# Kernel optimization log

Hardware: AMD Instinct MI355X
Metric: run time of the kernel (lower is better)

Reference implementation:

```python
import jax, jax.numpy as jnp
import numpy as np


def setup_inputs() -> dict:
    key = jax.random.key(0)
    k1, k2, k3 = jax.random.split(key, 3)
    S, B, H, D = 1024, 32, 512, 1024  # max_len, batch, bin_rnn_size, bin_rep_size
    hidden = jax.random.normal(k1, (2, B, H), dtype=jnp.float32)
    encoder_outputs = jax.random.normal(k2, (S, B, D), dtype=jnp.float32)
    # nn.Linear(D, D) params; scale W for numerically sane softmax logits
    W = jax.random.normal(k3, (D, D), dtype=jnp.float32) / np.float32(np.sqrt(D))
    b = jnp.zeros((D,), dtype=jnp.float32)
    return {"hidden": hidden, "encoder_outputs": encoder_outputs, "W": W, "b": b}


def reference(hidden, encoder_outputs, W, b):
    # method == 'general'
    B = hidden.shape[1]
    # torch.reshape((-1, B, 2H)).squeeze() == C-order flatten -> [B, 2H]
    h = hidden.reshape(B, -1)                                   # [B, D]
    energy = jnp.einsum('sbd,ed->sbe', encoder_outputs, W) + b  # Linear: x @ W.T + b
    # batch_product_luong + sum over features == contraction
    attn_energies = jnp.einsum('bd,sbd->bs', h, energy)         # [B, S]
    alpha = jax.nn.softmax(attn_energies, axis=1)[:, None, :]   # [B, 1, S]
    # alpha.bmm(encoder_outputs.transpose(0,1)) -> [B, 1, D]
    reps = jnp.einsum('bos,sbd->bod', alpha, encoder_outputs)
    return (reps, alpha)
```

## Files before the change

kernel.cpp:

```cpp
#include <hip/hip_runtime.h>

#define S 1024
#define B 32
#define D 1024
#define NCH 32
#define CH (S / NCH)
#define RPW (CH / 4)
#define NPAIR (RPW / 2)
#define ECH 8
#define EC 128

#define PG_OFF   0
#define G_OFF    (PG_OFF + ECH * B * D)
#define LOG_OFF  (G_OFF + B * D)
#define MARR_OFF (LOG_OFF + B * S)
#define LARR_OFF (MARR_OFF + NCH * B)
#define PACC_OFF (LARR_OFF + NCH * B)

__global__ __launch_bounds__(256) void kA(const float* __restrict__ hid,
                                          const float* __restrict__ W,
                                          float* __restrict__ ws) {
    const int tid = threadIdx.x;
    const int ec = blockIdx.x >> 5;
    const int dc = blockIdx.x & 31;
    __shared__ float h_sh[EC * 33];
    #pragma unroll
    for (int k = 0; k < (EC * B) / 256; ++k) {
        int lin = tid + k * 256;
        int b = lin >> 7;
        int e = lin & (EC - 1);
        h_sh[e * 33 + b] = hid[b * D + ec * EC + e];
    }
    __syncthreads();

    const int dq = tid & 7;
    const int b  = tid >> 3;
    const float4* W4 = (const float4*)W;
    float4 a4 = {0.f, 0.f, 0.f, 0.f};
    for (int e = 0; e < EC; ++e) {
        float h  = h_sh[e * 33 + b];
        float4 w = W4[((size_t)(ec * EC + e) * D + dc * 32) / 4 + dq];
        a4.x += h * w.x; a4.y += h * w.y; a4.z += h * w.z; a4.w += h * w.w;
    }
    float* pg = ws + PG_OFF;
    ((float4*)(pg + (size_t)(ec * B + b) * D + dc * 32))[dq] = a4;
}

__global__ __launch_bounds__(256) void kA2(float* __restrict__ ws) {
    const int idx = blockIdx.x * 256 + threadIdx.x;
    const float4* pg4 = (const float4*)(ws + PG_OFF);
    float4 s4 = {0.f, 0.f, 0.f, 0.f};
    #pragma unroll
    for (int ec = 0; ec < ECH; ++ec) {
        float4 v = pg4[(size_t)ec * (B * D / 4) + idx];
        s4.x += v.x; s4.y += v.y; s4.z += v.z; s4.w += v.w;
    }
    ((float4*)(ws + G_OFF))[idx] = s4;
}

__global__ __launch_bounds__(256) void kB(const float* __restrict__ enc,
                                          float* __restrict__ ws) {
    const int tid  = threadIdx.x;
    const int lane = tid & 63;
    const int wid  = tid >> 6;
    const int c    = blockIdx.x;
    const int b    = blockIdx.y;

    const float* g = ws + G_OFF;
    float* logits = ws + LOG_OFF;
    float* marr   = ws + MARR_OFF;
    float* larr   = ws + LARR_OFF;
    float* pacc   = ws + PACC_OFF;

    __shared__ float4 sacc[4 * 256];
    __shared__ float sm[4], sl[4];

    const float4* encb = (const float4*)enc;
    const int row0 = c * CH + wid * RPW;
    const size_t rstride = (size_t)B * (D / 4);
    size_t base = ((size_t)row0 * B + b) * (D / 4) + lane;

    float4 cur[8], nxt[8];
    #pragma unroll
    for (int j = 0; j < 4; ++j) {
        cur[j]     = encb[base + j * 64];
        cur[4 + j] = encb[base + rstride + j * 64];
    }
    #pragma unroll
    for (int j = 0; j < 4; ++j) {
        nxt[j]     = encb[base + 2 * rstride + j * 64];
        nxt[4 + j] = encb[base + 3 * rstride + j * 64];
    }
    float4 gv[4];
    #pragma unroll
    for (int j = 0; j < 4; ++j)
        gv[j] = ((const float4*)(g + b * D))[j * 64 + lane];

    float m = -3.0e38f, l = 0.f;
    float4 acc[4] = {{0,0,0,0},{0,0,0,0},{0,0,0,0},{0,0,0,0}};

    #pragma unroll
    for (int p = 0; p < NPAIR; ++p) {
        float pd0 = 0.f, pd1 = 0.f;
        #pragma unroll
        for (int j = 0; j < 4; ++j) {
            pd0 += cur[j].x * gv[j].x + cur[j].y * gv[j].y +
                   cur[j].z * gv[j].z + cur[j].w * gv[j].w;
            pd1 += cur[4+j].x * gv[j].x + cur[4+j].y * gv[j].y +
                   cur[4+j].z * gv[j].z + cur[4+j].w * gv[j].w;
        }
        #pragma unroll
        for (int off = 1; off < 64; off <<= 1) {
            pd0 += __shfl_xor(pd0, off, 64);
            pd1 += __shfl_xor(pd1, off, 64);
        }
        if (lane == 0) {
            logits[b * S + row0 + 2 * p]     = pd0;
            logits[b * S + row0 + 2 * p + 1] = pd1;
        }
        float mn  = fmaxf(m, pd0);
        float sc0 = __expf(m - mn);
        float pA  = __expf(pd0 - mn);
        float mn2 = fmaxf(mn, pd1);
        float sc1 = __expf(mn - mn2);
        float pB  = __expf(pd1 - mn2);
        float s01 = sc0 * sc1;
        float a0  = pA * sc1;
        l = l * s01 + a0 + pB;
        #pragma unroll
        for (int j = 0; j < 4; ++j) {
            acc[j].x = acc[j].x * s01 + a0 * cur[j].x + pB * cur[4+j].x;
            acc[j].y = acc[j].y * s01 + a0 * cur[j].y + pB * cur[4+j].y;
            acc[j].z = acc[j].z * s01 + a0 * cur[j].z + pB * cur[4+j].z;
            acc[j].w = acc[j].w * s01 + a0 * cur[j].w + pB * cur[4+j].w;
        }
        m = mn2;
        if (p + 1 < NPAIR) {
            #pragma unroll
            for (int j = 0; j < 8; ++j) cur[j] = nxt[j];
        }
        if (p + 2 < NPAIR) {
            size_t nb = base + (size_t)(2 * (p + 2)) * rstride;
            #pragma unroll
            for (int j = 0; j < 4; ++j) {
                nxt[j]     = encb[nb + j * 64];
                nxt[4 + j] = encb[nb + rstride + j * 64];
            }
        }
    }

    #pragma unroll
    for (int j = 0; j < 4; ++j) sacc[wid * 256 + j * 64 + lane] = acc[j];
    if (lane == 0) { sm[wid] = m; sl[wid] = l; }
    __syncthreads();
    float mg = fmaxf(fmaxf(sm[0], sm[1]), fmaxf(sm[2], sm[3]));
    float4 r = {0.f, 0.f, 0.f, 0.f};
    float lsum = 0.f;
    #pragma unroll
    for (int w = 0; w < 4; ++w) {
        float fw = __expf(sm[w] - mg);
        float4 a = sacc[w * 256 + wid * 64 + lane];
        r.x += a.x * fw; r.y += a.y * fw; r.z += a.z * fw; r.w += a.w * fw;
        lsum += sl[w] * fw;
    }
    ((float4*)pacc)[(size_t)(c * B + b) * (D / 4) + tid] = r;
    if (tid == 0) { marr[c * B + b] = mg; larr[c * B + b] = lsum; }
}

__global__ __launch_bounds__(256) void kC(float* __restrict__ out,
                                          const float* __restrict__ ws) {
    const int tid = threadIdx.x;
    const int q   = blockIdx.x;
    const int b   = blockIdx.y;
    const float* logits = ws + LOG_OFF;
    const float* marr   = ws + MARR_OFF;
    const float* larr   = ws + LARR_OFF;
    const float* pacc   = ws + PACC_OFF;

    __shared__ float shm[NCH], shl[NCH], shf[NCH];
    if (tid < NCH) { shm[tid] = marr[tid * B + b]; shl[tid] = larr[tid * B + b]; }
    __syncthreads();
    float mg = -3.0e38f;
    #pragma unroll
    for (int cc = 0; cc < NCH; ++cc) mg = fmaxf(mg, shm[cc]);
    if (tid < NCH) shf[tid] = __expf(shm[tid] - mg);
    __syncthreads();
    float lg = 0.f;
    #pragma unroll
    for (int cc = 0; cc < NCH; ++cc) lg += shl[cc] * shf[cc];
    const float inv = 1.f / lg;

    if (tid < 64) {
        const int d4 = q * 64 + tid;
        float4 racc = {0.f, 0.f, 0.f, 0.f};
        #pragma unroll 4
        for (int cc = 0; cc < NCH; ++cc) {
            float  fc = shf[cc];
            float4 v  = ((const float4*)pacc)[(size_t)(cc * B + b) * (D / 4) + d4];
            racc.x += v.x * fc; racc.y += v.y * fc;
            racc.z += v.z * fc; racc.w += v.w * fc;
        }
        float4 rep = {racc.x * inv, racc.y * inv, racc.z * inv, racc.w * inv};
        ((float4*)out)[b * (D / 4) + d4] = rep;
    }
    const int s = q * 256 + tid;
    out[B * D + b * S + s] = __expf(logits[b * S + s] - mg) * inv;
}

extern "C" void kernel_launch(void* const* d_in, const int* in_sizes, int n_in,
                              void* d_out, int out_size, void* d_ws, size_t ws_size,
                              hipStream_t stream) {
    const float* hid = (const float*)d_in[0];
    const float* enc = (const float*)d_in[1];
    const float* W   = (const float*)d_in[2];

    float* out = (float*)d_out;
    float* ws  = (float*)d_ws;

    kA<<<dim3(ECH * 32), 256, 0, stream>>>(hid, W, ws);
    kA2<<<dim3(32), 256, 0, stream>>>(ws);
    kB<<<dim3(NCH, B), 256, 0, stream>>>(enc, ws);
    kC<<<dim3(4, B), 256, 0, stream>>>(out, ws);
}
```

Before: 42.51 us.

## Fuse hidden-times-W GEMV and partial-sum reduction into one kernel

The split-K projection kernel and its separate reduction kernel are replaced by one kernel of 64 blocks with 128 threads. Each block loops over all 1024 input features in chunks of 128 staged through shared memory. This drops one launch and the write and read-back of the partial-sum buffer. In exchange the stage runs on far fewer threads, and each thread does a long serial loop, so latency hiding and parallelism in this stage drop sharply.

```diff
diff --git a/kernel.cpp b/kernel.cpp
--- a/kernel.cpp
+++ b/kernel.cpp
@@ -7,55 +7,36 @@
 #define CH (S / NCH)
 #define RPW (CH / 4)
 #define NPAIR (RPW / 2)
-#define ECH 8
-#define EC 128
-
-#define PG_OFF   0
-#define G_OFF    (PG_OFF + ECH * B * D)
+
+#define G_OFF    0
 #define LOG_OFF  (G_OFF + B * D)
 #define MARR_OFF (LOG_OFF + B * S)
 #define LARR_OFF (MARR_OFF + NCH * B)
 #define PACC_OFF (LARR_OFF + NCH * B)
 
-__global__ __launch_bounds__(256) void kA(const float* __restrict__ hid,
-                                          const float* __restrict__ W,
-                                          float* __restrict__ ws) {
+__global__ __launch_bounds__(128) void kAg(const float* __restrict__ hid,
+                                           const float* __restrict__ W,
+                                           float* __restrict__ ws) {
     const int tid = threadIdx.x;
-    const int ec = blockIdx.x >> 5;
-    const int dc = blockIdx.x & 31;
-    __shared__ float h_sh[EC * 33];
-    #pragma unroll
-    for (int k = 0; k < (EC * B) / 256; ++k) {
-        int lin = tid + k * 256;
-        int b = lin >> 7;
-        int e = lin & (EC - 1);
-        h_sh[e * 33 + b] = hid[b * D + ec * EC + e];
-    }
-    __syncthreads();
-
-    const int dq = tid & 7;
-    const int b  = tid >> 3;
+    const int dc  = blockIdx.x;
+    __shared__ float h_sh[128 * 33];
+    const int b  = tid >> 2;
+    const int dq = tid & 3;
     const float4* W4 = (const float4*)W;
     float4 a4 = {0.f, 0.f, 0.f, 0.f};
-    for (int e = 0; e < EC; ++e) {
-        float h  = h_sh[e * 33 + b];
-        float4 w = W4[((size_t)(ec * EC + e) * D + dc * 32) / 4 + dq];
-        a4.x += h * w.x; a4.y += h * w.y; a4.z += h * w.z; a4.w += h * w.w;
-    }
-    float* pg = ws + PG_OFF;
-    ((float4*)(pg + (size_t)(ec * B + b) * D + dc * 32))[dq] = a4;
-}
-
-__global__ __launch_bounds__(256) void kA2(float* __restrict__ ws) {
-    const int idx = blockIdx.x * 256 + threadIdx.x;
-    const float4* pg4 = (const float4*)(ws + PG_OFF);
-    float4 s4 = {0.f, 0.f, 0.f, 0.f};
-    #pragma unroll
-    for (int ec = 0; ec < ECH; ++ec) {
-        float4 v = pg4[(size_t)ec * (B * D / 4) + idx];
-        s4.x += v.x; s4.y += v.y; s4.z += v.z; s4.w += v.w;
-    }
-    ((float4*)(ws + G_OFF))[idx] = s4;
+    for (int ech = 0; ech < 8; ++ech) {
+        __syncthreads();
+        #pragma unroll
+        for (int k = 0; k < 32; ++k)
+            h_sh[tid * 33 + k] = hid[k * D + ech * 128 + tid];
+        __syncthreads();
+        for (int e = 0; e < 128; ++e) {
+            float  h = h_sh[e * 33 + b];
+            float4 w = W4[(size_t)(ech * 128 + e) * (D / 4) + dc * 4 + dq];
+            a4.x += h * w.x; a4.y += h * w.y; a4.z += h * w.z; a4.w += h * w.w;
+        }
+    }
+    ((float4*)(ws + G_OFF + b * D + dc * 16))[dq] = a4;
 }
 
 __global__ __launch_bounds__(256) void kB(const float* __restrict__ enc,
@@ -217,8 +198,7 @@
     float* out = (float*)d_out;
     float* ws  = (float*)d_ws;
 
-    kA<<<dim3(ECH * 32), 256, 0, stream>>>(hid, W, ws);
-    kA2<<<dim3(32), 256, 0, stream>>>(ws);
+    kAg<<<dim3(64), 128, 0, stream>>>(hid, W, ws);
     kB<<<dim3(NCH, B), 256, 0, stream>>>(enc, ws);
     kC<<<dim3(4, B), 256, 0, stream>>>(out, ws);
 }
```

Measured after the change: 90.82 us. 114% more time.
